# Performance work log

Measured on AMD Instinct MI355X. Metric: run time of the kernel, lower is better.

The kernel has to match this reference:

```python
import jax, jax.numpy as jnp
import numpy as np

DIM_HEADS = 64
NB_FEATURES = 256
KERNEL_EPS = 1e-4


def _gaussian_orthogonal_random_matrix(nb_rows, nb_cols, seed=0):
    # scaling == 1: rows scaled by sqrt(nb_cols); orthogonal QR blocks
    rng = np.random.RandomState(seed)
    nb_full_blocks = nb_rows // nb_cols
    blocks = []
    for _ in range(nb_full_blocks):
        unstructured = rng.randn(nb_cols, nb_cols)
        q, _ = np.linalg.qr(unstructured)
        blocks.append(q.T)
    rem = nb_rows - nb_full_blocks * nb_cols
    if rem > 0:
        unstructured = rng.randn(nb_cols, nb_cols)
        q, _ = np.linalg.qr(unstructured)
        blocks.append(q.T[:rem])
    final = np.concatenate(blocks, axis=0)
    multiplier = np.sqrt(float(nb_cols)) * np.ones((nb_rows,))
    return (multiplier[:, None] * final).astype(np.float32)


def setup_inputs() -> dict:
    key = jax.random.key(0)
    kq, kk, kv = jax.random.split(key, 3)
    b, h, n, d = 4, 16, 4096, DIM_HEADS
    q = jax.random.normal(kq, (b, h, n, d), dtype=jnp.float32)
    k = jax.random.normal(kk, (b, h, n, d), dtype=jnp.float32)
    v = jax.random.normal(kv, (b, h, n, d), dtype=jnp.float32)
    proj = jnp.asarray(_gaussian_orthogonal_random_matrix(NB_FEATURES, d))  # [m, d]
    return {"q": q, "k": k, "v": v, "proj": proj}


def _softmax_kernel(data, proj, is_query, eps=KERNEL_EPS):
    d = data.shape[-1]
    m = proj.shape[0]
    data_normalizer = d ** (-0.25)
    ratio = m ** (-0.5)
    # [b,h,n,m]
    data_dash = jnp.einsum('bhnd,md->bhnm', data_normalizer * data, proj)
    diag_data = jnp.sum(data ** 2, axis=-1, keepdims=True) * 0.5 * data_normalizer ** 2
    if is_query:
        stab = jax.lax.stop_gradient(jnp.max(data_dash, axis=-1, keepdims=True))
    else:
        stab = jax.lax.stop_gradient(jnp.max(data_dash, axis=(-1, -2), keepdims=True))
    return ratio * (jnp.exp(data_dash - diag_data - stab) + eps)


def _linear_attention(q, k, v):
    # q,k: [b,h,n,m] features; v: [b,h,n,e]
    k_cumsum = jnp.sum(k, axis=-2)                               # [b,h,m]
    D_inv = 1.0 / jnp.einsum('bhnm,bhm->bhn', q, k_cumsum)       # [b,h,n]
    context = jnp.einsum('bhnm,bhne->bhme', k, v)                # [b,h,m,e]
    return jnp.einsum('bhme,bhnm,bhn->bhne', context, q, D_inv)  # [b,h,n,e]


def reference(q, k, v, proj):
    q_prime = _softmax_kernel(q, proj, is_query=True)
    k_prime = _softmax_kernel(k, proj, is_query=False)
    return _linear_attention(q_prime, k_prime, v)
```

## Files before the change

kernel.cpp:

```cpp
#include <hip/hip_runtime.h>

#define SEQ 4096
#define CDN 0.35355339059327379f
#define DIAGC 0.0625f
#define KEPS 1e-4f

typedef _Float16 f16;
typedef f16 f16x8 __attribute__((ext_vector_type(8)));
typedef f16 f16x4 __attribute__((ext_vector_type(4)));
typedef float f32x4 __attribute__((ext_vector_type(4)));

#define MFMA16(a, b, c) __builtin_amdgcn_mfma_f32_16x16x32_f16(a, b, c, 0, 0, 0)

#define PSTR 72

__device__ __forceinline__ void stage_proj(const float* __restrict__ proj, f16* plds) {
  int t = threadIdx.x;
  int mrow = t >> 2;
  int cb = (t & 3) * 16;
#pragma unroll
  for (int p = 0; p < 4; ++p) {
    int m = mrow + p * 64;
    const float4* src = (const float4*)(proj + m * 64 + cb);
    f16* dst = plds + m * PSTR + cb;
#pragma unroll
    for (int i = 0; i < 4; ++i) {
      float4 v = src[i];
      f16x4 h = {(f16)v.x, (f16)v.y, (f16)v.z, (f16)v.w};
      *(f16x4*)(dst + i * 4) = h;
    }
  }
}

__device__ __forceinline__ f16x8 proj_frag(const f16* plds, int mtile, int ks, int lane) {
  int m = (lane & 15) + 16 * mtile;
  return *(const f16x8*)(plds + m * PSTR + ks * 32 + (lane >> 4) * 8);
}

__device__ __forceinline__ f16x8 pfrag32(const float* __restrict__ proj, int mt, int ks, int lane) {
  const float4* p = (const float4*)(proj + (size_t)(16 * mt + (lane & 15)) * 64 + ks * 32 + (lane >> 4) * 8);
  float4 a = p[0], b = p[1];
  f16x8 r = {(f16)a.x, (f16)a.y, (f16)a.z, (f16)a.w,
             (f16)b.x, (f16)b.y, (f16)b.z, (f16)b.w};
  return r;
}

__device__ __forceinline__ f16x8 row_frag(const float* __restrict__ base, int lane, int ks, float& sq) {
  const float4* p = (const float4*)(base + (size_t)(lane & 15) * 64 + ks * 32 + (lane >> 4) * 8);
  float4 a = p[0], b = p[1];
  sq += a.x*a.x + a.y*a.y + a.z*a.z + a.w*a.w + b.x*b.x + b.y*b.y + b.z*b.z + b.w*b.w;
  f16x8 r = {(f16)(a.x*CDN), (f16)(a.y*CDN), (f16)(a.z*CDN), (f16)(a.w*CDN),
             (f16)(b.x*CDN), (f16)(b.y*CDN), (f16)(b.z*CDN), (f16)(b.w*CDN)};
  return r;
}

__device__ __forceinline__ f16x8 row_frag_ns(const float* __restrict__ base, int lane, int ks) {
  const float4* p = (const float4*)(base + (size_t)(lane & 15) * 64 + ks * 32 + (lane >> 4) * 8);
  float4 a = p[0], b = p[1];
  f16x8 r = {(f16)(a.x*CDN), (f16)(a.y*CDN), (f16)(a.z*CDN), (f16)(a.w*CDN),
             (f16)(b.x*CDN), (f16)(b.y*CDN), (f16)(b.z*CDN), (f16)(b.w*CDN)};
  return r;
}

__global__ __launch_bounds__(256, 2) void k1_stab(
    const float* __restrict__ kk, const float* __restrict__ proj,
    float* __restrict__ ws_stab) {
  __shared__ float wred[4];
  int bh = blockIdx.x >> 3, blk = blockIdx.x & 7;
  int w = threadIdx.x >> 6, lane = threadIdx.x & 63;
  f16x8 pf[16][2];
#pragma unroll
  for (int mt = 0; mt < 16; ++mt) {
    pf[mt][0] = pfrag32(proj, mt, 0, lane);
    pf[mt][1] = pfrag32(proj, mt, 1, lane);
  }
  const float* kbh = kk + (size_t)bh * SEQ * 64;
  float rmax = -1e30f;
#pragma unroll 1
  for (int it = 0; it < 8; ++it) {
    int n0 = blk * 512 + it * 64 + w * 16;
    f16x8 b0 = row_frag_ns(kbh + (size_t)n0 * 64, lane, 0);
    f16x8 b1 = row_frag_ns(kbh + (size_t)n0 * 64, lane, 1);
#pragma unroll
    for (int mt = 0; mt < 16; ++mt) {
      f32x4 acc = {0.f, 0.f, 0.f, 0.f};
      acc = MFMA16(pf[mt][0], b0, acc);
      acc = MFMA16(pf[mt][1], b1, acc);
      rmax = fmaxf(rmax, fmaxf(fmaxf(acc[0], acc[1]), fmaxf(acc[2], acc[3])));
    }
  }
#pragma unroll
  for (int m = 1; m < 64; m <<= 1) rmax = fmaxf(rmax, __shfl_xor(rmax, m, 64));
  if (lane == 0) wred[w] = rmax;
  __syncthreads();
  if (threadIdx.x == 0)
    ws_stab[bh * 8 + blk] = fmaxf(fmaxf(wred[0], wred[1]), fmaxf(wred[2], wred[3]));
}

#define VSTR 72

__device__ __forceinline__ void stage_vT(const float* __restrict__ vbh, int n, int e8, int nl, f16* dst) {
  const float4* vp = (const float4*)(vbh + (size_t)n * 64 + e8);
  float4 a = vp[0], b = vp[1];
  dst[(e8 + 0) * VSTR + nl] = (f16)a.x;
  dst[(e8 + 1) * VSTR + nl] = (f16)a.y;
  dst[(e8 + 2) * VSTR + nl] = (f16)a.z;
  dst[(e8 + 3) * VSTR + nl] = (f16)a.w;
  dst[(e8 + 4) * VSTR + nl] = (f16)b.x;
  dst[(e8 + 5) * VSTR + nl] = (f16)b.y;
  dst[(e8 + 6) * VSTR + nl] = (f16)b.z;
  dst[(e8 + 7) * VSTR + nl] = (f16)b.w;
}

__global__ __launch_bounds__(512, 4) void k2_ctx(
    const float* __restrict__ kk, const float* __restrict__ vv,
    const float* __restrict__ proj, const float* __restrict__ ws_stab,
    float* __restrict__ ctx_part, float* __restrict__ kcum_part) {
  __shared__ __align__(16) f16 vt[2][64 * VSTR];
  __shared__ __align__(16) f16 pht[8][16 * 40];
  __shared__ __align__(16) float diag_s[8][32];
  __shared__ float red2[4][16];
  int bh = blockIdx.x & 63, rest = blockIdx.x >> 6;
  int mc = rest & 3, ns = rest >> 2;
  int w = threadIdx.x >> 6, lane = threadIdx.x & 63;
  int q4 = lane >> 4, l15 = lane & 15;
  int mtl = w & 3, nsub = w >> 2;
  float stab = -1e30f;
#pragma unroll
  for (int i = 0; i < 8; ++i) stab = fmaxf(stab, ws_stab[bh * 8 + i]);
  f16x8 pa0 = pfrag32(proj, mc * 4 + mtl, 0, lane);
  f16x8 pa1 = pfrag32(proj, mc * 4 + mtl, 1, lane);
  const float* kbh = kk + (size_t)bh * SEQ * 64;
  const float* vbh = vv + (size_t)bh * SEQ * 64;
  f32x4 actx[4];
  f32x4 akc = {0.f, 0.f, 0.f, 0.f};
#pragma unroll
  for (int i = 0; i < 4; ++i) actx[i] = (f32x4){0.f, 0.f, 0.f, 0.f};
  f16x8 ones = {(f16)1.f, (f16)1.f, (f16)1.f, (f16)1.f,
                (f16)1.f, (f16)1.f, (f16)1.f, (f16)1.f};
  int nl = threadIdx.x & 63, e8 = (threadIdx.x >> 6) * 8;
  int nbase = ns * 2048;
  stage_vT(vbh, nbase + nl, e8, nl, &vt[0][0]);
  __syncthreads();
#pragma unroll 1
  for (int it = 0; it < 32; ++it) {
    int n0 = nbase + it * 64;
    if (it < 31) stage_vT(vbh, n0 + 64 + nl, e8, nl, &vt[(it & 1) ^ 1][0]);
    const f16* vcur = &vt[it & 1][0];
    f16x8 ak[2][2];
    float dg[2];
#pragma unroll
    for (int nt = 0; nt < 2; ++nt) {
      float sq = 0.f;
      const float* kb = kbh + (size_t)(n0 + nsub * 32 + nt * 16) * 64;
      ak[nt][0] = row_frag(kb, lane, 0, sq);
      ak[nt][1] = row_frag(kb, lane, 1, sq);
      sq += __shfl_xor(sq, 16, 64);
      sq += __shfl_xor(sq, 32, 64);
      dg[nt] = sq * DIAGC;
    }
    if (lane < 16) { diag_s[w][lane] = dg[0]; diag_s[w][16 + lane] = dg[1]; }
#pragma unroll
    for (int nt = 0; nt < 2; ++nt) {
      f32x4 acc = {0.f, 0.f, 0.f, 0.f};
      acc = MFMA16(ak[nt][0], pa0, acc);
      acc = MFMA16(ak[nt][1], pa1, acc);
      float4 dgv = ((const float4*)&diag_s[w][0])[nt * 4 + q4];
      f16x4 ph;
      ph[0] = (f16)(__expf(acc[0] - dgv.x - stab) + KEPS);
      ph[1] = (f16)(__expf(acc[1] - dgv.y - stab) + KEPS);
      ph[2] = (f16)(__expf(acc[2] - dgv.z - stab) + KEPS);
      ph[3] = (f16)(__expf(acc[3] - dgv.w - stab) + KEPS);
      *(f16x4*)(&pht[w][l15 * 40 + nt * 16 + q4 * 4]) = ph;
    }
    f16x8 bv[4];
#pragma unroll
    for (int et = 0; et < 4; ++et)
      bv[et] = *(const f16x8*)(vcur + (l15 + 16 * et) * VSTR + nsub * 32 + q4 * 8);
    f16x8 aph = *(const f16x8*)(&pht[w][l15 * 40 + q4 * 8]);
    akc = MFMA16(aph, ones, akc);
#pragma unroll
    for (int et = 0; et < 4; ++et) actx[et] = MFMA16(aph, bv[et], actx[et]);
    __syncthreads();
  }
  float* red = (float*)&vt[0][0];
  if (nsub == 1) {
#pragma unroll
    for (int et = 0; et < 4; ++et)
#pragma unroll
      for (int r = 0; r < 4; ++r)
        red[mtl * 1024 + (q4 * 4 + r) * 64 + l15 + 16 * et] = actx[et][r];
    if (l15 == 0) {
#pragma unroll
      for (int r = 0; r < 4; ++r) red2[mtl][q4 * 4 + r] = akc[r];
    }
  }
  __syncthreads();
  if (nsub == 0) {
    float* cp = ctx_part + (((size_t)bh * 2 + ns) * 256 + mc * 64 + mtl * 16) * 64;
#pragma unroll
    for (int et = 0; et < 4; ++et)
#pragma unroll
      for (int r = 0; r < 4; ++r)
        cp[(size_t)(q4 * 4 + r) * 64 + l15 + 16 * et] =
            actx[et][r] + red[mtl * 1024 + (q4 * 4 + r) * 64 + l15 + 16 * et];
    if (l15 == 0) {
#pragma unroll
      for (int r = 0; r < 4; ++r)
        kcum_part[((size_t)bh * 2 + ns) * 256 + mc * 64 + mtl * 16 + q4 * 4 + r] =
            akc[r] + red2[mtl][q4 * 4 + r];
    }
  }
}

__global__ __launch_bounds__(256) void k2c_red(
    const float* __restrict__ ctx_part, const float* __restrict__ kcum_part,
    float* __restrict__ ws_kcum, f16* __restrict__ ws_ctxT) {
  __shared__ float tile[64 * 65];
  int bh = blockIdx.x & 63, mq = blockIdx.x >> 6;
  int t = threadIdx.x;
  const float* c0 = ctx_part + (((size_t)bh * 2 + 0) * 256 + mq * 64) * 64;
  const float* c1 = ctx_part + (((size_t)bh * 2 + 1) * 256 + mq * 64) * 64;
#pragma unroll
  for (int i = 0; i < 16; ++i) {
    int idx = t + i * 256;
    int ml = idx >> 6, e = idx & 63;
    tile[ml * 65 + e] = c0[idx] + c1[idx];
  }
  if (t < 64) {
    ws_kcum[bh * 256 + mq * 64 + t] =
        kcum_part[((size_t)bh * 2 + 0) * 256 + mq * 64 + t] +
        kcum_part[((size_t)bh * 2 + 1) * 256 + mq * 64 + t];
  }
  __syncthreads();
  f16* ct = ws_ctxT + (size_t)bh * 16384 + mq * 64;
  int mj = t & 63, eg = t >> 6;
#pragma unroll
  for (int i = 0; i < 16; ++i) {
    int e = eg + i * 4;
    ct[(size_t)e * 256 + mj] = (f16)tile[mj * 65 + e];
  }
}

#define CSTR 264

__global__ __launch_bounds__(256, 2) void k3_out(
    const float* __restrict__ qq, const float* __restrict__ proj,
    const float* __restrict__ ws_kcum, const f16* __restrict__ ws_ctxT,
    float* __restrict__ out) {
  __shared__ __align__(16) f16 plds[256 * PSTR];
  __shared__ __align__(16) f16 ctx_l[64 * CSTR];
  __shared__ __align__(16) f16 phq[4][16 * 72];
  int bh = blockIdx.x >> 4, blk = blockIdx.x & 15;
  int t = threadIdx.x;
  stage_proj(proj, plds);
  {
    const f16* cb = ws_ctxT + (size_t)bh * 16384;
#pragma unroll
    for (int i = 0; i < 8; ++i) {
      int c = t + i * 256;
      int e = c >> 5, mo = (c & 31) * 8;
      *(f16x8*)(ctx_l + e * CSTR + mo) = *(const f16x8*)(cb + e * 256 + mo);
    }
  }
  int w = t >> 6, lane = t & 63;
  int q4 = lane >> 4, l15 = lane & 15;
  const float* qbh = qq + (size_t)bh * SEQ * 64;
  const float4* kcv = (const float4*)(ws_kcum + bh * 256);
  float* obh = out + (size_t)bh * SEQ * 64;
  __syncthreads();
#pragma unroll 1
  for (int it = 0; it < 4; ++it) {
    int n0 = blk * 256 + w * 64 + it * 16;
    float sq = 0.f;
    f16x8 bq0 = row_frag(qbh + (size_t)n0 * 64, lane, 0, sq);
    f16x8 bq1 = row_frag(qbh + (size_t)n0 * 64, lane, 1, sq);
    sq += __shfl_xor(sq, 16, 64);
    sq += __shfl_xor(sq, 32, 64);
    float diag = sq * DIAGC;
    f32x4 dd[16];
#pragma unroll
    for (int mt = 0; mt < 16; ++mt) {
      f32x4 acc = {0.f, 0.f, 0.f, 0.f};
      acc = MFMA16(proj_frag(plds, mt, 0, lane), bq0, acc);
      acc = MFMA16(proj_frag(plds, mt, 1, lane), bq1, acc);
      dd[mt] = acc;
    }
    float st = -1e30f;
#pragma unroll
    for (int mt = 0; mt < 16; ++mt)
      st = fmaxf(st, fmaxf(fmaxf(dd[mt][0], dd[mt][1]), fmaxf(dd[mt][2], dd[mt][3])));
    st = fmaxf(st, __shfl_xor(st, 16, 64));
    st = fmaxf(st, __shfl_xor(st, 32, 64));
    float dacc = 0.f;
    f32x4 ao[4];
#pragma unroll
    for (int r = 0; r < 4; ++r) ao[r] = (f32x4){0.f, 0.f, 0.f, 0.f};
#pragma unroll
    for (int qtr = 0; qtr < 4; ++qtr) {
#pragma unroll
      for (int m2 = 0; m2 < 4; ++m2) {
        int mt = qtr * 4 + m2;
        float4 kc = kcv[mt * 4 + q4];
        float e0 = __expf(dd[mt][0] - diag - st) + KEPS;
        float e1 = __expf(dd[mt][1] - diag - st) + KEPS;
        float e2 = __expf(dd[mt][2] - diag - st) + KEPS;
        float e3 = __expf(dd[mt][3] - diag - st) + KEPS;
        dacc += e0 * kc.x + e1 * kc.y + e2 * kc.z + e3 * kc.w;
        f16x4 ph;
        ph[0] = (f16)e0; ph[1] = (f16)e1; ph[2] = (f16)e2; ph[3] = (f16)e3;
        *(f16x4*)(&phq[w][l15 * 72 + m2 * 16 + q4 * 4]) = ph;
      }
#pragma unroll
      for (int kl = 0; kl < 2; ++kl) {
        int ks2 = qtr * 2 + kl;
        f16x8 bph = *(const f16x8*)(&phq[w][l15 * 72 + kl * 32 + q4 * 8]);
#pragma unroll
        for (int rte = 0; rte < 4; ++rte) {
          f16x8 act = *(const f16x8*)(ctx_l + (l15 + 16 * rte) * CSTR + ks2 * 32 + q4 * 8);
          ao[rte] = MFMA16(act, bph, ao[rte]);
        }
      }
    }
    dacc += __shfl_xor(dacc, 16, 64);
    dacc += __shfl_xor(dacc, 32, 64);
    float dinv = 1.0f / dacc;
#pragma unroll
    for (int rte = 0; rte < 4; ++rte) {
      float4 o;
      o.x = ao[rte][0] * dinv;
      o.y = ao[rte][1] * dinv;
      o.z = ao[rte][2] * dinv;
      o.w = ao[rte][3] * dinv;
      *(float4*)(obh + (size_t)(n0 + l15) * 64 + rte * 16 + q4 * 4) = o;
    }
  }
}

extern "C" void kernel_launch(void* const* d_in, const int* in_sizes, int n_in,
                              void* d_out, int out_size, void* d_ws, size_t ws_size,
                              hipStream_t stream) {
  const float* q = (const float*)d_in[0];
  const float* k = (const float*)d_in[1];
  const float* v = (const float*)d_in[2];
  const float* proj = (const float*)d_in[3];
  float* out = (float*)d_out;
  float* ws = (float*)d_ws;
  float* ws_stab = ws;
  float* ws_kcum = ws + 1024;
  f16*   ws_ctxT = (f16*)(ws + 17408);
  float* ctx_part  = out;
  float* kcum_part = out + 4194304;
  k1_stab<<<512, 256, 0, stream>>>(k, proj, ws_stab);
  k2_ctx<<<512, 512, 0, stream>>>(k, v, proj, ws_stab, ctx_part, kcum_part);
  k2c_red<<<256, 256, 0, stream>>>(ctx_part, kcum_part, ws_kcum, ws_ctxT);
  k3_out<<<1024, 256, 0, stream>>>(q, proj, ws_kcum, ws_ctxT, out);
}
```

Baseline: 478.2 us.

## Replace separate key-max pass with online rescaled stabilizer in context kernel

Removes the k1_stab kernel, which made a full extra pass over K just to find the global max. The context kernel now tracks a running max and rescales its accumulators when the max grows. The reduction kernel merges partials with exp(M_i - S) factors and adds the eps term analytically, using sum(v) and the sequence length. The sequence split is doubled to 1024 blocks, and k3 caches kcum in LDS. The cost is extra per-iteration wave reductions and rescales, plus fp16 rounding of un-eps'd features, which may change accuracy slightly.

```diff
diff --git a/kernel.cpp b/kernel.cpp
--- a/kernel.cpp
+++ b/kernel.cpp
@@ -52,49 +52,6 @@
   f16x8 r = {(f16)(a.x*CDN), (f16)(a.y*CDN), (f16)(a.z*CDN), (f16)(a.w*CDN),
              (f16)(b.x*CDN), (f16)(b.y*CDN), (f16)(b.z*CDN), (f16)(b.w*CDN)};
   return r;
-}
-
-__device__ __forceinline__ f16x8 row_frag_ns(const float* __restrict__ base, int lane, int ks) {
-  const float4* p = (const float4*)(base + (size_t)(lane & 15) * 64 + ks * 32 + (lane >> 4) * 8);
-  float4 a = p[0], b = p[1];
-  f16x8 r = {(f16)(a.x*CDN), (f16)(a.y*CDN), (f16)(a.z*CDN), (f16)(a.w*CDN),
-             (f16)(b.x*CDN), (f16)(b.y*CDN), (f16)(b.z*CDN), (f16)(b.w*CDN)};
-  return r;
-}
-
-__global__ __launch_bounds__(256, 2) void k1_stab(
-    const float* __restrict__ kk, const float* __restrict__ proj,
-    float* __restrict__ ws_stab) {
-  __shared__ float wred[4];
-  int bh = blockIdx.x >> 3, blk = blockIdx.x & 7;
-  int w = threadIdx.x >> 6, lane = threadIdx.x & 63;
-  f16x8 pf[16][2];
-#pragma unroll
-  for (int mt = 0; mt < 16; ++mt) {
-    pf[mt][0] = pfrag32(proj, mt, 0, lane);
-    pf[mt][1] = pfrag32(proj, mt, 1, lane);
-  }
-  const float* kbh = kk + (size_t)bh * SEQ * 64;
-  float rmax = -1e30f;
-#pragma unroll 1
-  for (int it = 0; it < 8; ++it) {
-    int n0 = blk * 512 + it * 64 + w * 16;
-    f16x8 b0 = row_frag_ns(kbh + (size_t)n0 * 64, lane, 0);
-    f16x8 b1 = row_frag_ns(kbh + (size_t)n0 * 64, lane, 1);
-#pragma unroll
-    for (int mt = 0; mt < 16; ++mt) {
-      f32x4 acc = {0.f, 0.f, 0.f, 0.f};
-      acc = MFMA16(pf[mt][0], b0, acc);
-      acc = MFMA16(pf[mt][1], b1, acc);
-      rmax = fmaxf(rmax, fmaxf(fmaxf(acc[0], acc[1]), fmaxf(acc[2], acc[3])));
-    }
-  }
-#pragma unroll
-  for (int m = 1; m < 64; m <<= 1) rmax = fmaxf(rmax, __shfl_xor(rmax, m, 64));
-  if (lane == 0) wred[w] = rmax;
-  __syncthreads();
-  if (threadIdx.x == 0)
-    ws_stab[bh * 8 + blk] = fmaxf(fmaxf(wred[0], wred[1]), fmaxf(wred[2], wred[3]));
 }
 
 #define VSTR 72
@@ -114,20 +71,19 @@
 
 __global__ __launch_bounds__(512, 4) void k2_ctx(
     const float* __restrict__ kk, const float* __restrict__ vv,
-    const float* __restrict__ proj, const float* __restrict__ ws_stab,
-    float* __restrict__ ctx_part, float* __restrict__ kcum_part) {
+    const float* __restrict__ proj,
+    float* __restrict__ ctx_part, float* __restrict__ kcum_part,
+    float* __restrict__ stabm, float* __restrict__ vs_part) {
   __shared__ __align__(16) f16 vt[2][64 * VSTR];
   __shared__ __align__(16) f16 pht[8][16 * 40];
   __shared__ __align__(16) float diag_s[8][32];
   __shared__ float red2[4][16];
+  __shared__ float stabs[8];
   int bh = blockIdx.x & 63, rest = blockIdx.x >> 6;
   int mc = rest & 3, ns = rest >> 2;
   int w = threadIdx.x >> 6, lane = threadIdx.x & 63;
   int q4 = lane >> 4, l15 = lane & 15;
   int mtl = w & 3, nsub = w >> 2;
-  float stab = -1e30f;
-#pragma unroll
-  for (int i = 0; i < 8; ++i) stab = fmaxf(stab, ws_stab[bh * 8 + i]);
   f16x8 pa0 = pfrag32(proj, mc * 4 + mtl, 0, lane);
   f16x8 pa1 = pfrag32(proj, mc * 4 + mtl, 1, lane);
   const float* kbh = kk + (size_t)bh * SEQ * 64;
@@ -136,16 +92,18 @@
   f32x4 akc = {0.f, 0.f, 0.f, 0.f};
 #pragma unroll
   for (int i = 0; i < 4; ++i) actx[i] = (f32x4){0.f, 0.f, 0.f, 0.f};
+  float vsacc[4] = {0.f, 0.f, 0.f, 0.f};
+  float M = -1e30f;
   f16x8 ones = {(f16)1.f, (f16)1.f, (f16)1.f, (f16)1.f,
                 (f16)1.f, (f16)1.f, (f16)1.f, (f16)1.f};
   int nl = threadIdx.x & 63, e8 = (threadIdx.x >> 6) * 8;
-  int nbase = ns * 2048;
+  int nbase = ns * 1024;
   stage_vT(vbh, nbase + nl, e8, nl, &vt[0][0]);
   __syncthreads();
 #pragma unroll 1
-  for (int it = 0; it < 32; ++it) {
+  for (int it = 0; it < 16; ++it) {
     int n0 = nbase + it * 64;
-    if (it < 31) stage_vT(vbh, n0 + 64 + nl, e8, nl, &vt[(it & 1) ^ 1][0]);
+    if (it < 15) stage_vT(vbh, n0 + 64 + nl, e8, nl, &vt[(it & 1) ^ 1][0]);
     const f16* vcur = &vt[it & 1][0];
     f16x8 ak[2][2];
     float dg[2];
@@ -160,28 +118,73 @@
       dg[nt] = sq * DIAGC;
     }
     if (lane < 16) { diag_s[w][lane] = dg[0]; diag_s[w][16 + lane] = dg[1]; }
+    f32x4 accv[2];
 #pragma unroll
     for (int nt = 0; nt < 2; ++nt) {
-      f32x4 acc = {0.f, 0.f, 0.f, 0.f};
-      acc = MFMA16(ak[nt][0], pa0, acc);
-      acc = MFMA16(ak[nt][1], pa1, acc);
+      f32x4 a = {0.f, 0.f, 0.f, 0.f};
+      a = MFMA16(ak[nt][0], pa0, a);
+      a = MFMA16(ak[nt][1], pa1, a);
+      accv[nt] = a;
+    }
+    float tm = fmaxf(fmaxf(fmaxf(accv[0][0], accv[0][1]), fmaxf(accv[0][2], accv[0][3])),
+                     fmaxf(fmaxf(accv[1][0], accv[1][1]), fmaxf(accv[1][2], accv[1][3])));
+#pragma unroll
+    for (int m = 1; m < 64; m <<= 1) tm = fmaxf(tm, __shfl_xor(tm, m, 64));
+    if (tm > M) {
+      float rs = __expf(M - tm);
+      akc *= rs;
+#pragma unroll
+      for (int et = 0; et < 4; ++et) actx[et] *= rs;
+      M = tm;
+    }
+#pragma unroll
+    for (int nt = 0; nt < 2; ++nt) {
       float4 dgv = ((const float4*)&diag_s[w][0])[nt * 4 + q4];
       f16x4 ph;
-      ph[0] = (f16)(__expf(acc[0] - dgv.x - stab) + KEPS);
-      ph[1] = (f16)(__expf(acc[1] - dgv.y - stab) + KEPS);
-      ph[2] = (f16)(__expf(acc[2] - dgv.z - stab) + KEPS);
-      ph[3] = (f16)(__expf(acc[3] - dgv.w - stab) + KEPS);
+      ph[0] = (f16)__expf(accv[nt][0] - dgv.x - M);
+      ph[1] = (f16)__expf(accv[nt][1] - dgv.y - M);
+      ph[2] = (f16)__expf(accv[nt][2] - dgv.z - M);
+      ph[3] = (f16)__expf(accv[nt][3] - dgv.w - M);
       *(f16x4*)(&pht[w][l15 * 40 + nt * 16 + q4 * 4]) = ph;
     }
     f16x8 bv[4];
 #pragma unroll
     for (int et = 0; et < 4; ++et)
       bv[et] = *(const f16x8*)(vcur + (l15 + 16 * et) * VSTR + nsub * 32 + q4 * 8);
+    if (mc == 0 && mtl == 0) {
+#pragma unroll
+      for (int et = 0; et < 4; ++et) {
+        float s = 0.f;
+#pragma unroll
+        for (int j = 0; j < 8; ++j) s += (float)bv[et][j];
+        vsacc[et] += s;
+      }
+    }
     f16x8 aph = *(const f16x8*)(&pht[w][l15 * 40 + q4 * 8]);
     akc = MFMA16(aph, ones, akc);
 #pragma unroll
     for (int et = 0; et < 4; ++et) actx[et] = MFMA16(aph, bv[et], actx[et]);
     __syncthreads();
+  }
+  if (lane == 0) stabs[w] = M;
+  __syncthreads();
+  float Mp = stabs[w ^ 4];
+  float Mt = fmaxf(M, Mp);
+  {
+    float sc = __expf(M - Mt);
+    akc *= sc;
+#pragma unroll
+    for (int et = 0; et < 4; ++et) actx[et] *= sc;
+  }
+  if (mc == 0 && mtl == 0) {
+#pragma unroll
+    for (int et = 0; et < 4; ++et) {
+      float s = vsacc[et];
+      s += __shfl_xor(s, 16, 64);
+      s += __shfl_xor(s, 32, 64);
+      if (lane < 16)
+        vs_part[(size_t)bh * 512 + (ns * 2 + nsub) * 64 + lane + 16 * et] = s;
+    }
   }
   float* red = (float*)&vt[0][0];
   if (nsub == 1) {
@@ -197,7 +200,7 @@
   }
   __syncthreads();
   if (nsub == 0) {
-    float* cp = ctx_part + (((size_t)bh * 2 + ns) * 256 + mc * 64 + mtl * 16) * 64;
+    float* cp = ctx_part + (((size_t)bh * 4 + ns) * 256 + mc * 64 + mtl * 16) * 64;
 #pragma unroll
     for (int et = 0; et < 4; ++et)
 #pragma unroll
@@ -207,30 +210,55 @@
     if (l15 == 0) {
 #pragma unroll
       for (int r = 0; r < 4; ++r)
-        kcum_part[((size_t)bh * 2 + ns) * 256 + mc * 64 + mtl * 16 + q4 * 4 + r] =
+        kcum_part[((size_t)bh * 4 + ns) * 256 + mc * 64 + mtl * 16 + q4 * 4 + r] =
             akc[r] + red2[mtl][q4 * 4 + r];
     }
+    if (lane == 0) stabm[(size_t)bh * 64 + ns * 16 + mc * 4 + mtl] = Mt;
   }
 }
 
 __global__ __launch_bounds__(256) void k2c_red(
     const float* __restrict__ ctx_part, const float* __restrict__ kcum_part,
+    const float* __restrict__ stabm, const float* __restrict__ vs_part,
     float* __restrict__ ws_kcum, f16* __restrict__ ws_ctxT) {
   __shared__ float tile[64 * 65];
+  __shared__ float sred[64];
+  __shared__ float vsum_l[64];
+  __shared__ float fac[4][4];
   int bh = blockIdx.x & 63, mq = blockIdx.x >> 6;
   int t = threadIdx.x;
-  const float* c0 = ctx_part + (((size_t)bh * 2 + 0) * 256 + mq * 64) * 64;
-  const float* c1 = ctx_part + (((size_t)bh * 2 + 1) * 256 + mq * 64) * 64;
+  if (t < 64) {
+    sred[t] = stabm[(size_t)bh * 64 + t];
+    float vs = 0.f;
+#pragma unroll
+    for (int i = 0; i < 8; ++i) vs += vs_part[(size_t)bh * 512 + i * 64 + t];
+    vsum_l[t] = vs;
+  }
+  __syncthreads();
+  float S = -1e30f;
+#pragma unroll
+  for (int i = 0; i < 64; ++i) S = fmaxf(S, sred[i]);
+  if (t < 16) fac[t >> 2][t & 3] = __expf(sred[(t >> 2) * 16 + mq * 4 + (t & 3)] - S);
+  __syncthreads();
+  const float* cp = ctx_part + ((size_t)bh * 4 * 256 + mq * 64) * 64;
 #pragma unroll
   for (int i = 0; i < 16; ++i) {
     int idx = t + i * 256;
     int ml = idx >> 6, e = idx & 63;
-    tile[ml * 65 + e] = c0[idx] + c1[idx];
+    int tl = ml >> 4;
+    float acc = KEPS * vsum_l[e];
+#pragma unroll
+    for (int ns = 0; ns < 4; ++ns)
+      acc += fac[ns][tl] * cp[(size_t)ns * 16384 + idx];
+    tile[ml * 65 + e] = acc;
   }
   if (t < 64) {
-    ws_kcum[bh * 256 + mq * 64 + t] =
-        kcum_part[((size_t)bh * 2 + 0) * 256 + mq * 64 + t] +
-        kcum_part[((size_t)bh * 2 + 1) * 256 + mq * 64 + t];
+    int tl = t >> 4;
+    float acc = KEPS * 4096.f;
+#pragma unroll
+    for (int ns = 0; ns < 4; ++ns)
+      acc += fac[ns][tl] * kcum_part[((size_t)bh * 4 + ns) * 256 + mq * 64 + t];
+    ws_kcum[bh * 256 + mq * 64 + t] = acc;
   }
   __syncthreads();
   f16* ct = ws_ctxT + (size_t)bh * 16384 + mq * 64;
@@ -251,9 +279,11 @@
   __shared__ __align__(16) f16 plds[256 * PSTR];
   __shared__ __align__(16) f16 ctx_l[64 * CSTR];
   __shared__ __align__(16) f16 phq[4][16 * 72];
+  __shared__ __align__(16) float kcl[256];
   int bh = blockIdx.x >> 4, blk = blockIdx.x & 15;
   int t = threadIdx.x;
   stage_proj(proj, plds);
+  kcl[t] = ws_kcum[bh * 256 + t];
   {
     const f16* cb = ws_ctxT + (size_t)bh * 16384;
 #pragma unroll
@@ -266,7 +296,6 @@
   int w = t >> 6, lane = t & 63;
   int q4 = lane >> 4, l15 = lane & 15;
   const float* qbh = qq + (size_t)bh * SEQ * 64;
-  const float4* kcv = (const float4*)(ws_kcum + bh * 256);
   float* obh = out + (size_t)bh * SEQ * 64;
   __syncthreads();
 #pragma unroll 1
@@ -301,7 +330,7 @@
 #pragma unroll
       for (int m2 = 0; m2 < 4; ++m2) {
         int mt = qtr * 4 + m2;
-        float4 kc = kcv[mt * 4 + q4];
+        float4 kc = ((const float4*)kcl)[mt * 4 + q4];
         float e0 = __expf(dd[mt][0] - diag - st) + KEPS;
         float e1 = __expf(dd[mt][1] - diag - st) + KEPS;
         float e2 = __expf(dd[mt][2] - diag - st) + KEPS;
@@ -346,13 +375,13 @@
   const float* proj = (const float*)d_in[3];
   float* out = (float*)d_out;
   float* ws = (float*)d_ws;
-  float* ws_stab = ws;
   float* ws_kcum = ws + 1024;
   f16*   ws_ctxT = (f16*)(ws + 17408);
   float* ctx_part  = out;
   float* kcum_part = out + 4194304;
-  k1_stab<<<512, 256, 0, stream>>>(k, proj, ws_stab);
-  k2_ctx<<<512, 512, 0, stream>>>(k, v, proj, ws_stab, ctx_part, kcum_part);
-  k2c_red<<<256, 256, 0, stream>>>(ctx_part, kcum_part, ws_kcum, ws_ctxT);
+  float* stabm     = out + 4259840;
+  float* vs_part   = out + 4263936;
+  k2_ctx<<<1024, 512, 0, stream>>>(k, v, proj, ctx_part, kcum_part, stabm, vs_part);
+  k2c_red<<<256, 256, 0, stream>>>(ctx_part, kcum_part, stabm, vs_part, ws_kcum, ws_ctxT);
   k3_out<<<1024, 256, 0, stream>>>(q, proj, ws_kcum, ws_ctxT, out);
 }
```

Measured after the change: 455.8 us. 1.05x faster.
